# Optimization experiments

Measured on AMD Instinct MI355X. Metric: run time of the kernel, lower is better.

The kernel has to match this reference:

```python
import jax, jax.numpy as jnp
import numpy as np

B, T, D, H = 4, 2048, 1024, 16


def setup_inputs() -> dict:
    key = jax.random.key(0)
    ks = jax.random.split(key, 5)
    s = 0.02  # keep activations sane
    return {
        "x": jax.random.normal(ks[0], (B, T, D), jnp.float32),
        "Wq": jax.random.normal(ks[1], (D, D), jnp.float32) * s,
        "bq": jnp.zeros((D,), jnp.float32),
        "Wk": jax.random.normal(ks[2], (D, D), jnp.float32) * s,
        "bk": jnp.zeros((D,), jnp.float32),
        "Wv": jax.random.normal(ks[3], (D, D), jnp.float32) * s,
        "bv": jnp.zeros((D,), jnp.float32),
        "Wo": jax.random.normal(ks[4], (D, D), jnp.float32) * s,
        "bo": jnp.zeros((D,), jnp.float32),
    }


def _split_heads(t):  # (B,T,D) -> (B,H,T,d)
    b, s, d = t.shape
    return t.reshape(b, s, H, d // H).transpose(0, 2, 1, 3)


def reference(x, Wq, bq, Wk, bk, Wv, bv, Wo, bo):
    d_k = D // H
    q = _split_heads(x @ Wq + bq)  # (B,H,T,d)
    k = _split_heads(x @ Wk + bk)
    v = _split_heads(x @ Wv + bv)
    # scaled dot-product similarities (B,H,T,T)
    scores = jnp.einsum("bhqd,bhkd->bhqk", q, k) / jnp.sqrt(jnp.asarray(d_k, x.dtype))
    # causal mask: masked_fill(tril==0, -inf)
    causal = jnp.tril(jnp.ones((T, T), bool))
    scores = jnp.where(causal, scores, -jnp.inf)
    attn = jax.nn.softmax(scores, axis=-1)
    ctx = jnp.einsum("bhqk,bhkd->bhqd", attn, v)  # (B,H,T,d)
    ctx = ctx.transpose(0, 2, 1, 3).reshape(x.shape[0], T, D)
    return ctx @ Wo + bo
```

## Files before the change

kernel.cpp:

```cpp
#include <hip/hip_runtime.h>
#include <hip/hip_bf16.h>

typedef unsigned short u16;
typedef __attribute__((ext_vector_type(8))) short bf16x8;
typedef __attribute__((ext_vector_type(4))) short bf16x4;
typedef __attribute__((ext_vector_type(4))) float f32x4;

#define DD 1024
#define TT 2048
#define HH 16
#define BB 4
#define DK 64
#define MM 8192

#define QSCALE 0.180336880f

__device__ __forceinline__ u16 f2b(float x) {
  __hip_bfloat16 h = __float2bfloat16(x);
  return *reinterpret_cast<u16*>(&h);
}

__device__ __forceinline__ unsigned pk2(float a, float b) {
  float2 t; t.x = a; t.y = b;
  __hip_bfloat162 h = __float22bfloat162_rn(t);
  union { __hip_bfloat162 h; unsigned u; } cv;
  cv.h = h;
  return cv.u;
}

#define GLD16(gp, lp)                                                         \
  __builtin_amdgcn_global_load_lds(                                           \
      (const __attribute__((address_space(1))) unsigned int*)(gp),            \
      (__attribute__((address_space(3))) unsigned int*)(lp), 16, 0, 0)

__global__ __launch_bounds__(256) void cast_bf16_kernel(
    const float* __restrict__ src, u16* __restrict__ dst, int n) {
  int i = (blockIdx.x * 256 + threadIdx.x) * 4;
  if (i + 3 < n) {
    float4 v = *reinterpret_cast<const float4*>(src + i);
    ushort4 o;
    o.x = f2b(v.x); o.y = f2b(v.y); o.z = f2b(v.z); o.w = f2b(v.w);
    *reinterpret_cast<ushort4*>(dst + i) = o;
  }
}

__global__ __launch_bounds__(256) void transpose_cast_kernel(
    const float* __restrict__ W0, const float* __restrict__ W1,
    const float* __restrict__ W2, const float* __restrict__ W3,
    u16* __restrict__ O0, u16* __restrict__ O1,
    u16* __restrict__ O2, u16* __restrict__ O3) {
  const float* W; u16* O;
  switch (blockIdx.z) {
    case 0: W = W0; O = O0; break;
    case 1: W = W1; O = O1; break;
    case 2: W = W2; O = O2; break;
    default: W = W3; O = O3; break;
  }
  __shared__ float tile[32][33];
  int tx = threadIdx.x, ty = threadIdx.y;
  int bx = blockIdx.x * 32;
  int by = blockIdx.y * 32;
#pragma unroll
  for (int j = 0; j < 4; j++)
    tile[ty + j * 8][tx] = W[(size_t)(by + ty + j * 8) * DD + bx + tx];
  __syncthreads();
#pragma unroll
  for (int j = 0; j < 4; j++)
    O[(size_t)(bx + ty + j * 8) * DD + by + tx] = f2b(tile[tx][ty + j * 8]);
}

__global__ __launch_bounds__(256) void gemm_qkv_kernel(
    const u16* __restrict__ A,
    const u16* __restrict__ WtQ, const u16* __restrict__ WtK,
    const u16* __restrict__ WtV,
    const float* __restrict__ bq, const float* __restrict__ bk,
    const float* __restrict__ bv,
    u16* __restrict__ Qo, u16* __restrict__ Ko, u16* __restrict__ Vo) {
  __shared__ __align__(16) u16 As[128 * 32];
  __shared__ __align__(16) u16 Bs[128 * 32];
  __shared__ __align__(16) u16 Vs[128 * 136];
  int z = blockIdx.z;
  const u16* Bt = (z == 0) ? WtQ : ((z == 1) ? WtK : WtV);
  const float* bias = (z == 0) ? bq : ((z == 1) ? bk : bv);
  int tid = threadIdx.x;
  int wave = tid >> 6, lane = tid & 63;
  int quad = lane >> 4, l16 = lane & 15;
  int m0 = blockIdx.x * 128, n0 = blockIdx.y * 128;
  int wm = (wave >> 1) * 64, wn = (wave & 1) * 64;

  f32x4 acc[4][4];
#pragma unroll
  for (int i = 0; i < 4; i++)
#pragma unroll
    for (int j = 0; j < 4; j++) acc[i][j] = (f32x4){0.f, 0.f, 0.f, 0.f};

  for (int k0 = 0; k0 < DD; k0 += 32) {
#pragma unroll
    for (int c = 0; c < 2; c++) {
      int idx = tid * 8 + c * 2048;
      int row = idx >> 5, kk = idx & 31;
      GLD16(A + (size_t)(m0 + row) * DD + k0 + kk, As + idx);
      GLD16(Bt + (size_t)(n0 + row) * DD + k0 + kk, Bs + idx);
    }
    __syncthreads();
    bf16x8 af[4], bfr[4];
#pragma unroll
    for (int mb = 0; mb < 4; mb++)
      af[mb] = *reinterpret_cast<const bf16x8*>(&As[(wm + mb * 16 + l16) * 32 + quad * 8]);
#pragma unroll
    for (int nb = 0; nb < 4; nb++)
      bfr[nb] = *reinterpret_cast<const bf16x8*>(&Bs[(wn + nb * 16 + l16) * 32 + quad * 8]);
#pragma unroll
    for (int mb = 0; mb < 4; mb++)
#pragma unroll
      for (int nb = 0; nb < 4; nb++)
        acc[mb][nb] = __builtin_amdgcn_mfma_f32_16x16x32_bf16(
            af[mb], bfr[nb], acc[mb][nb], 0, 0, 0);
    __syncthreads();
  }

  if (z == 2) {
#pragma unroll
    for (int mb = 0; mb < 4; mb++)
#pragma unroll
      for (int nb = 0; nb < 4; nb++) {
        int col = wn + nb * 16 + l16;
        float bv2 = bias[n0 + col];
#pragma unroll
        for (int r = 0; r < 4; r++) {
          int row = wm + mb * 16 + quad * 4 + r;
          Vs[col * 136 + row] = f2b(acc[mb][nb][r] + bv2);
        }
      }
    __syncthreads();
    int b = m0 >> 11;
    int tloc = m0 & 2047;
#pragma unroll
    for (int i = 0; i < 8; i++) {
      int idx = tid * 8 + i * 2048;
      int row = idx >> 7, col = idx & 127;
      uint4 v = *reinterpret_cast<const uint4*>(&Vs[row * 136 + col]);
      int ncol = n0 + row, h = ncol >> 6, dd = ncol & 63;
      *reinterpret_cast<uint4*>(
          Vo + (((size_t)(b * HH + h) * DK) + dd) * TT + tloc + col) = v;
    }
    return;
  }

  u16* outp = (z == 0) ? Qo : Ko;
  float scale = (z == 0) ? QSCALE : 1.0f;
#pragma unroll
  for (int mb = 0; mb < 4; mb++) {
#pragma unroll
    for (int nb = 0; nb < 4; nb++) {
      int col = n0 + wn + nb * 16 + l16;
      float bv2 = bias[col];
#pragma unroll
      for (int r = 0; r < 4; r++) {
        int row = m0 + wm + mb * 16 + quad * 4 + r;
        float val = (acc[mb][nb][r] + bv2) * scale;
        int hh = col >> 6, dd = col & 63;
        int b = row >> 11, t = row & 2047;
        outp[(((size_t)(b * HH + hh) * TT) + t) * DK + dd] = f2b(val);
      }
    }
  }
}

__global__ __launch_bounds__(256) void gemm_out_kernel(
    const u16* __restrict__ A, const u16* __restrict__ Bt,
    const float* __restrict__ bias, float* __restrict__ outp) {
  __shared__ __align__(16) u16 As[128 * 32];
  __shared__ __align__(16) u16 Bs[128 * 32];
  int tid = threadIdx.x;
  int wave = tid >> 6, lane = tid & 63;
  int quad = lane >> 4, l16 = lane & 15;
  int m0 = blockIdx.x * 128, n0 = blockIdx.y * 128;
  int wm = (wave >> 1) * 64, wn = (wave & 1) * 64;

  f32x4 acc[4][4];
#pragma unroll
  for (int i = 0; i < 4; i++)
#pragma unroll
    for (int j = 0; j < 4; j++) acc[i][j] = (f32x4){0.f, 0.f, 0.f, 0.f};

  for (int k0 = 0; k0 < DD; k0 += 32) {
#pragma unroll
    for (int c = 0; c < 2; c++) {
      int idx = tid * 8 + c * 2048;
      int row = idx >> 5, kk = idx & 31;
      GLD16(A + (size_t)(m0 + row) * DD + k0 + kk, As + idx);
      GLD16(Bt + (size_t)(n0 + row) * DD + k0 + kk, Bs + idx);
    }
    __syncthreads();
    bf16x8 af[4], bfr[4];
#pragma unroll
    for (int mb = 0; mb < 4; mb++)
      af[mb] = *reinterpret_cast<const bf16x8*>(&As[(wm + mb * 16 + l16) * 32 + quad * 8]);
#pragma unroll
    for (int nb = 0; nb < 4; nb++)
      bfr[nb] = *reinterpret_cast<const bf16x8*>(&Bs[(wn + nb * 16 + l16) * 32 + quad * 8]);
#pragma unroll
    for (int mb = 0; mb < 4; mb++)
#pragma unroll
      for (int nb = 0; nb < 4; nb++)
        acc[mb][nb] = __builtin_amdgcn_mfma_f32_16x16x32_bf16(
            af[mb], bfr[nb], acc[mb][nb], 0, 0, 0);
    __syncthreads();
  }

#pragma unroll
  for (int mb = 0; mb < 4; mb++) {
#pragma unroll
    for (int nb = 0; nb < 4; nb++) {
      int col = n0 + wn + nb * 16 + l16;
      float bv = bias[col];
#pragma unroll
      for (int r = 0; r < 4; r++) {
        int row = m0 + wm + mb * 16 + quad * 4 + r;
        outp[(size_t)row * DD + col] = acc[mb][nb][r] + bv;
      }
    }
  }
}

__global__ __launch_bounds__(512, 4) void attn_kernel(
    const u16* __restrict__ Q, const u16* __restrict__ K,
    const u16* __restrict__ VT, u16* __restrict__ ctx) {
  __shared__ __align__(16) u16 Ks[2][64][72];
  __shared__ __align__(16) u16 Vt[2][64][72];

  int tid = threadIdx.x;
  int wave = tid >> 6, lane = tid & 63;
  int quad = lane >> 4, l16 = lane & 15;
  int bid = blockIdx.x;
  int bh = bid & 63;
  int qt = 15 - (bid >> 6);
  int b = bh >> 4, h = bh & 15;
  const u16* Qh = Q + (size_t)bh * TT * DK;
  const u16* Kh = K + (size_t)bh * TT * DK;
  const u16* Vh = VT + (size_t)bh * DK * TT;
  int sidx = tid * 8;

  int ktmax = 2 * qt + 1;
  int dtile = 2 * qt + (wave >> 2);
  int qrl = (wave * 16 + l16) & 63;

  const u16* qrow = Qh + (size_t)(qt * 128 + wave * 16 + l16) * DK + quad * 8;
  bf16x8 qf0 = *reinterpret_cast<const bf16x8*>(qrow);
  bf16x8 qf1 = *reinterpret_cast<const bf16x8*>(qrow + 32);

  uint4 kpre = *reinterpret_cast<const uint4*>(Kh + sidx);
  uint4 vpre = *reinterpret_cast<const uint4*>(Vh + (size_t)(sidx >> 6) * TT + (sidx & 63));
  *reinterpret_cast<uint4*>(&Ks[0][sidx >> 6][sidx & 63]) = kpre;
  *reinterpret_cast<uint4*>(&Vt[0][sidx >> 6][sidx & 63]) = vpre;
  __syncthreads();

  f32x4 oacc[4];
#pragma unroll
  for (int dt = 0; dt < 4; dt++) oacc[dt] = (f32x4){0.f, 0.f, 0.f, 0.f};
  f32x4 lacc = (f32x4){0.f, 0.f, 0.f, 0.f};
  const bf16x4 ones = (bf16x4){0x3F80, 0x3F80, 0x3F80, 0x3F80};

  for (int kt = 0; kt <= ktmax; kt++) {
    int cur = kt & 1, nxt = cur ^ 1;
    bool more = kt < ktmax;
    if (more) {
      kpre = *reinterpret_cast<const uint4*>(Kh + (size_t)(kt + 1) * 4096 + sidx);
      vpre = *reinterpret_cast<const uint4*>(
          Vh + (size_t)(sidx >> 6) * TT + (kt + 1) * 64 + (sidx & 63));
    }

    if (kt <= dtile) {
      f32x4 sacc[4];
#pragma unroll
      for (int kb = 0; kb < 4; kb++) sacc[kb] = (f32x4){0.f, 0.f, 0.f, 0.f};
#pragma unroll
      for (int kb = 0; kb < 4; kb++) {
        bf16x8 kf0 = *reinterpret_cast<const bf16x8*>(&Ks[cur][kb * 16 + l16][quad * 8]);
        bf16x8 kf1 = *reinterpret_cast<const bf16x8*>(&Ks[cur][kb * 16 + l16][32 + quad * 8]);
        sacc[kb] = __builtin_amdgcn_mfma_f32_16x16x32_bf16(kf0, qf0, sacc[kb], 0, 0, 0);
        sacc[kb] = __builtin_amdgcn_mfma_f32_16x16x32_bf16(kf1, qf1, sacc[kb], 0, 0, 0);
      }

      if (kt == dtile) {
#pragma unroll
        for (int kb = 0; kb < 4; kb++)
#pragma unroll
          for (int r = 0; r < 4; r++)
            if (kb * 16 + quad * 4 + r > qrl) sacc[kb][r] = -__builtin_inff();
      }

#pragma unroll
      for (int kb = 0; kb < 4; kb++) {
        float p0 = __builtin_amdgcn_exp2f(sacc[kb][0]);
        float p1 = __builtin_amdgcn_exp2f(sacc[kb][1]);
        float p2 = __builtin_amdgcn_exp2f(sacc[kb][2]);
        float p3 = __builtin_amdgcn_exp2f(sacc[kb][3]);
        union { unsigned u[2]; bf16x4 v; } pk;
        pk.u[0] = pk2(p0, p1);
        pk.u[1] = pk2(p2, p3);
        lacc = __builtin_amdgcn_mfma_f32_16x16x16bf16_1k(pk.v, ones, lacc, 0, 0, 0);
#pragma unroll
        for (int dt = 0; dt < 4; dt++) {
          bf16x4 vf = *reinterpret_cast<const bf16x4*>(
              &Vt[cur][dt * 16 + l16][kb * 16 + quad * 4]);
          oacc[dt] = __builtin_amdgcn_mfma_f32_16x16x16bf16_1k(pk.v, vf, oacc[dt], 0, 0, 0);
        }
      }
    }

    if (more) {
      *reinterpret_cast<uint4*>(&Ks[nxt][sidx >> 6][sidx & 63]) = kpre;
      *reinterpret_cast<uint4*>(&Vt[nxt][sidx >> 6][sidx & 63]) = vpre;
    }
    __syncthreads();
  }

  f32x4 inv;
#pragma unroll
  for (int r = 0; r < 4; r++) inv[r] = 1.0f / lacc[r];

  u16* Obuf = &Ks[0][0][0];
#pragma unroll
  for (int dt = 0; dt < 4; dt++)
#pragma unroll
    for (int r = 0; r < 4; r++)
      Obuf[(wave * 16 + quad * 4 + r) * 72 + dt * 16 + l16] =
          f2b(oacc[dt][r] * inv[r]);
  asm volatile("s_waitcnt lgkmcnt(0)" ::: "memory");
#pragma unroll
  for (int i = 0; i < 2; i++) {
    int idx = lane * 8 + i * 512;
    int row = idx >> 6, colc = idx & 63;
    uint4 v = *reinterpret_cast<const uint4*>(&Obuf[(wave * 16 + row) * 72 + colc]);
    int t = qt * 128 + wave * 16 + row;
    *reinterpret_cast<uint4*>(
        ctx + ((size_t)(b * TT + t)) * DD + h * DK + colc) = v;
  }
}

extern "C" void kernel_launch(void* const* d_in, const int* in_sizes, int n_in,
                              void* d_out, int out_size, void* d_ws, size_t ws_size,
                              hipStream_t stream) {
  const float* x  = (const float*)d_in[0];
  const float* Wq = (const float*)d_in[1];
  const float* bq = (const float*)d_in[2];
  const float* Wk = (const float*)d_in[3];
  const float* bk = (const float*)d_in[4];
  const float* Wv = (const float*)d_in[5];
  const float* bv = (const float*)d_in[6];
  const float* Wo = (const float*)d_in[7];
  const float* bo = (const float*)d_in[8];
  float* out = (float*)d_out;

  char* ws = (char*)d_ws;
  size_t off = 0;
  u16* xb  = (u16*)(ws + off); off += (size_t)MM * DD * 2;
  u16* wtq = (u16*)(ws + off); off += (size_t)DD * DD * 2;
  u16* wtk = (u16*)(ws + off); off += (size_t)DD * DD * 2;
  u16* wtv = (u16*)(ws + off); off += (size_t)DD * DD * 2;
  u16* wto = (u16*)(ws + off); off += (size_t)DD * DD * 2;
  u16* Qb  = (u16*)(ws + off); off += (size_t)MM * DD * 2;
  u16* Kb  = (u16*)(ws + off); off += (size_t)MM * DD * 2;
  u16* VTb = (u16*)(ws + off); off += (size_t)MM * DD * 2;
  u16* ctx = (u16*)(ws + off); off += (size_t)MM * DD * 2;

  {
    int n = MM * DD;
    cast_bf16_kernel<<<n / 1024, 256, 0, stream>>>(x, xb, n);
  }
  {
    dim3 grid(DD / 32, DD / 32, 4);
    dim3 block(32, 8);
    transpose_cast_kernel<<<grid, block, 0, stream>>>(Wq, Wk, Wv, Wo, wtq, wtk, wtv, wto);
  }
  {
    dim3 grid(MM / 128, DD / 128, 3);
    gemm_qkv_kernel<<<grid, 256, 0, stream>>>(xb, wtq, wtk, wtv, bq, bk, bv,
                                              Qb, Kb, VTb);
  }
  {
    attn_kernel<<<1024, 512, 0, stream>>>(Qb, Kb, VTb, ctx);
  }
  {
    dim3 grid(MM / 128, DD / 128);
    gemm_out_kernel<<<grid, 256, 0, stream>>>(ctx, wto, bo, out);
  }
}
```

Measured before the change: 264.0 us.

## Use K=64 XOR-swizzled LDS tiles and split QKV GEMM into QK and V kernels

Doubles the GEMM K-step from 32 to 64 and stores LDS tiles with an XOR swizzle on the column index, so each sync pair covers twice the MFMA work and LDS reads avoid bank conflicts. The QKV kernel is split into a QK kernel and a separate V kernel. The V kernel reuses the A/B tile memory for its transpose buffer, which keeps LDS per block low, and launch bounds ask for 4 blocks per CU. This adds one kernel launch and loses no work, but the loop stays single-buffered.

```diff
diff --git a/kernel.cpp b/kernel.cpp
--- a/kernel.cpp
+++ b/kernel.cpp
@@ -69,19 +69,44 @@
     O[(size_t)(bx + ty + j * 8) * DD + by + tx] = f2b(tile[tx][ty + j * 8]);
 }
 
-__global__ __launch_bounds__(256) void gemm_qkv_kernel(
+#define GEMM_STAGE(Aptr, Bptr, Asl, Bsl)                                      \
+  _Pragma("unroll") for (int c = 0; c < 4; c++) {                             \
+    int idx = tid * 8 + c * 2048;                                             \
+    int row = idx >> 6, ck = idx & 63;                                        \
+    int src = ck ^ ((row & 7) << 3);                                          \
+    GLD16(Aptr + (size_t)(m0 + row) * DD + k0 + src, Asl + idx);              \
+    GLD16(Bptr + (size_t)(n0 + row) * DD + k0 + src, Bsl + idx);              \
+  }
+
+#define GEMM_MFMA(Asl, Bsl)                                                   \
+  _Pragma("unroll") for (int half = 0; half < 2; half++) {                    \
+    bf16x8 af[4], bfr[4];                                                     \
+    _Pragma("unroll") for (int mb = 0; mb < 4; mb++) {                        \
+      int r = wm + mb * 16 + l16;                                             \
+      af[mb] = *reinterpret_cast<const bf16x8*>(                              \
+          &Asl[r * 64 + ((half * 32 + quad * 8) ^ ((r & 7) << 3))]);          \
+    }                                                                         \
+    _Pragma("unroll") for (int nb = 0; nb < 4; nb++) {                        \
+      int r = wn + nb * 16 + l16;                                             \
+      bfr[nb] = *reinterpret_cast<const bf16x8*>(                             \
+          &Bsl[r * 64 + ((half * 32 + quad * 8) ^ ((r & 7) << 3))]);          \
+    }                                                                         \
+    _Pragma("unroll") for (int mb = 0; mb < 4; mb++)                          \
+      _Pragma("unroll") for (int nb = 0; nb < 4; nb++)                        \
+          acc[mb][nb] = __builtin_amdgcn_mfma_f32_16x16x32_bf16(              \
+              af[mb], bfr[nb], acc[mb][nb], 0, 0, 0);                         \
+  }
+
+__global__ __launch_bounds__(256, 4) void gemm_qk_kernel(
     const u16* __restrict__ A,
     const u16* __restrict__ WtQ, const u16* __restrict__ WtK,
-    const u16* __restrict__ WtV,
     const float* __restrict__ bq, const float* __restrict__ bk,
-    const float* __restrict__ bv,
-    u16* __restrict__ Qo, u16* __restrict__ Ko, u16* __restrict__ Vo) {
-  __shared__ __align__(16) u16 As[128 * 32];
-  __shared__ __align__(16) u16 Bs[128 * 32];
-  __shared__ __align__(16) u16 Vs[128 * 136];
+    u16* __restrict__ Qo, u16* __restrict__ Ko) {
+  __shared__ __align__(16) u16 As[128 * 64];
+  __shared__ __align__(16) u16 Bs[128 * 64];
   int z = blockIdx.z;
-  const u16* Bt = (z == 0) ? WtQ : ((z == 1) ? WtK : WtV);
-  const float* bias = (z == 0) ? bq : ((z == 1) ? bk : bv);
+  const u16* Bt = z ? WtK : WtQ;
+  const float* bias = z ? bk : bq;
   int tid = threadIdx.x;
   int wave = tid >> 6, lane = tid & 63;
   int quad = lane >> 4, l16 = lane & 15;
@@ -94,61 +119,15 @@
 #pragma unroll
     for (int j = 0; j < 4; j++) acc[i][j] = (f32x4){0.f, 0.f, 0.f, 0.f};
 
-  for (int k0 = 0; k0 < DD; k0 += 32) {
-#pragma unroll
-    for (int c = 0; c < 2; c++) {
-      int idx = tid * 8 + c * 2048;
-      int row = idx >> 5, kk = idx & 31;
-      GLD16(A + (size_t)(m0 + row) * DD + k0 + kk, As + idx);
-      GLD16(Bt + (size_t)(n0 + row) * DD + k0 + kk, Bs + idx);
-    }
-    __syncthreads();
-    bf16x8 af[4], bfr[4];
-#pragma unroll
-    for (int mb = 0; mb < 4; mb++)
-      af[mb] = *reinterpret_cast<const bf16x8*>(&As[(wm + mb * 16 + l16) * 32 + quad * 8]);
-#pragma unroll
-    for (int nb = 0; nb < 4; nb++)
-      bfr[nb] = *reinterpret_cast<const bf16x8*>(&Bs[(wn + nb * 16 + l16) * 32 + quad * 8]);
-#pragma unroll
-    for (int mb = 0; mb < 4; mb++)
-#pragma unroll
-      for (int nb = 0; nb < 4; nb++)
-        acc[mb][nb] = __builtin_amdgcn_mfma_f32_16x16x32_bf16(
-            af[mb], bfr[nb], acc[mb][nb], 0, 0, 0);
-    __syncthreads();
-  }
-
-  if (z == 2) {
-#pragma unroll
-    for (int mb = 0; mb < 4; mb++)
-#pragma unroll
-      for (int nb = 0; nb < 4; nb++) {
-        int col = wn + nb * 16 + l16;
-        float bv2 = bias[n0 + col];
-#pragma unroll
-        for (int r = 0; r < 4; r++) {
-          int row = wm + mb * 16 + quad * 4 + r;
-          Vs[col * 136 + row] = f2b(acc[mb][nb][r] + bv2);
-        }
-      }
-    __syncthreads();
-    int b = m0 >> 11;
-    int tloc = m0 & 2047;
-#pragma unroll
-    for (int i = 0; i < 8; i++) {
-      int idx = tid * 8 + i * 2048;
-      int row = idx >> 7, col = idx & 127;
-      uint4 v = *reinterpret_cast<const uint4*>(&Vs[row * 136 + col]);
-      int ncol = n0 + row, h = ncol >> 6, dd = ncol & 63;
-      *reinterpret_cast<uint4*>(
-          Vo + (((size_t)(b * HH + h) * DK) + dd) * TT + tloc + col) = v;
-    }
-    return;
-  }
-
-  u16* outp = (z == 0) ? Qo : Ko;
-  float scale = (z == 0) ? QSCALE : 1.0f;
+  for (int k0 = 0; k0 < DD; k0 += 64) {
+    GEMM_STAGE(A, Bt, As, Bs)
+    __syncthreads();
+    GEMM_MFMA(As, Bs)
+    __syncthreads();
+  }
+
+  u16* outp = z ? Ko : Qo;
+  float scale = z ? 1.0f : QSCALE;
 #pragma unroll
   for (int mb = 0; mb < 4; mb++) {
 #pragma unroll
@@ -167,11 +146,13 @@
   }
 }
 
-__global__ __launch_bounds__(256) void gemm_out_kernel(
+__global__ __launch_bounds__(256, 4) void gemm_v_kernel(
     const u16* __restrict__ A, const u16* __restrict__ Bt,
-    const float* __restrict__ bias, float* __restrict__ outp) {
-  __shared__ __align__(16) u16 As[128 * 32];
-  __shared__ __align__(16) u16 Bs[128 * 32];
+    const float* __restrict__ bias, u16* __restrict__ Vo) {
+  __shared__ __align__(16) u16 smem[17408];
+  u16* As = smem;
+  u16* Bs = smem + 8192;
+  u16* Vs = smem;
   int tid = threadIdx.x;
   int wave = tid >> 6, lane = tid & 63;
   int quad = lane >> 4, l16 = lane & 15;
@@ -184,28 +165,60 @@
 #pragma unroll
     for (int j = 0; j < 4; j++) acc[i][j] = (f32x4){0.f, 0.f, 0.f, 0.f};
 
-  for (int k0 = 0; k0 < DD; k0 += 32) {
-#pragma unroll
-    for (int c = 0; c < 2; c++) {
-      int idx = tid * 8 + c * 2048;
-      int row = idx >> 5, kk = idx & 31;
-      GLD16(A + (size_t)(m0 + row) * DD + k0 + kk, As + idx);
-      GLD16(Bt + (size_t)(n0 + row) * DD + k0 + kk, Bs + idx);
-    }
-    __syncthreads();
-    bf16x8 af[4], bfr[4];
-#pragma unroll
-    for (int mb = 0; mb < 4; mb++)
-      af[mb] = *reinterpret_cast<const bf16x8*>(&As[(wm + mb * 16 + l16) * 32 + quad * 8]);
-#pragma unroll
-    for (int nb = 0; nb < 4; nb++)
-      bfr[nb] = *reinterpret_cast<const bf16x8*>(&Bs[(wn + nb * 16 + l16) * 32 + quad * 8]);
-#pragma unroll
-    for (int mb = 0; mb < 4; mb++)
-#pragma unroll
-      for (int nb = 0; nb < 4; nb++)
-        acc[mb][nb] = __builtin_amdgcn_mfma_f32_16x16x32_bf16(
-            af[mb], bfr[nb], acc[mb][nb], 0, 0, 0);
+  for (int k0 = 0; k0 < DD; k0 += 64) {
+    GEMM_STAGE(A, Bt, As, Bs)
+    __syncthreads();
+    GEMM_MFMA(As, Bs)
+    __syncthreads();
+  }
+
+#pragma unroll
+  for (int mb = 0; mb < 4; mb++)
+#pragma unroll
+    for (int nb = 0; nb < 4; nb++) {
+      int col = wn + nb * 16 + l16;
+      float bv2 = bias[n0 + col];
+#pragma unroll
+      for (int r = 0; r < 4; r++) {
+        int row = wm + mb * 16 + quad * 4 + r;
+        Vs[col * 136 + row] = f2b(acc[mb][nb][r] + bv2);
+      }
+    }
+  __syncthreads();
+  int b = m0 >> 11;
+  int tloc = m0 & 2047;
+#pragma unroll
+  for (int i = 0; i < 8; i++) {
+    int idx = tid * 8 + i * 2048;
+    int row = idx >> 7, col = idx & 127;
+    uint4 v = *reinterpret_cast<const uint4*>(&Vs[row * 136 + col]);
+    int ncol = n0 + row, h = ncol >> 6, dd = ncol & 63;
+    *reinterpret_cast<uint4*>(
+        Vo + (((size_t)(b * HH + h) * DK) + dd) * TT + tloc + col) = v;
+  }
+}
+
+__global__ __launch_bounds__(256, 4) void gemm_out_kernel(
+    const u16* __restrict__ A, const u16* __restrict__ Bt,
+    const float* __restrict__ bias, float* __restrict__ outp) {
+  __shared__ __align__(16) u16 As[128 * 64];
+  __shared__ __align__(16) u16 Bs[128 * 64];
+  int tid = threadIdx.x;
+  int wave = tid >> 6, lane = tid & 63;
+  int quad = lane >> 4, l16 = lane & 15;
+  int m0 = blockIdx.x * 128, n0 = blockIdx.y * 128;
+  int wm = (wave >> 1) * 64, wn = (wave & 1) * 64;
+
+  f32x4 acc[4][4];
+#pragma unroll
+  for (int i = 0; i < 4; i++)
+#pragma unroll
+    for (int j = 0; j < 4; j++) acc[i][j] = (f32x4){0.f, 0.f, 0.f, 0.f};
+
+  for (int k0 = 0; k0 < DD; k0 += 64) {
+    GEMM_STAGE(A, Bt, As, Bs)
+    __syncthreads();
+    GEMM_MFMA(As, Bs)
     __syncthreads();
   }
 
@@ -376,9 +389,12 @@
     transpose_cast_kernel<<<grid, block, 0, stream>>>(Wq, Wk, Wv, Wo, wtq, wtk, wtv, wto);
   }
   {
-    dim3 grid(MM / 128, DD / 128, 3);
-    gemm_qkv_kernel<<<grid, 256, 0, stream>>>(xb, wtq, wtk, wtv, bq, bk, bv,
-                                              Qb, Kb, VTb);
+    dim3 grid(MM / 128, DD / 128, 2);
+    gemm_qk_kernel<<<grid, 256, 0, stream>>>(xb, wtq, wtk, bq, bk, Qb, Kb);
+  }
+  {
+    dim3 grid(MM / 128, DD / 128);
+    gemm_v_kernel<<<grid, 256, 0, stream>>>(xb, wtv, bv, VTb);
   }
   {
     attn_kernel<<<1024, 512, 0, stream>>>(Qb, Kb, VTb, ctx);
```

New measurement: 248.8 us. -5.7%, faster.
